# Performance work log

Measured on AMD Instinct MI355X. Metric: run time of the kernel, lower is better.

## Reference

```python
import jax, jax.numpy as jnp
import numpy as np

N_HEAD = 16

def setup_inputs() -> dict:
    key = jax.random.key(0)
    k1, k2, k3, k4, k5 = jax.random.split(key, 5)
    B, S, D = 2, 2048, 1024
    return {
        "hidden_states": jax.random.normal(k1, (B, S, D), jnp.float32),
        "w_attn": jax.random.normal(k2, (D, 3 * D), jnp.float32) * 0.02,
        "b_attn": jax.random.normal(k3, (3 * D,), jnp.float32) * 0.02,
        "w_proj": jax.random.normal(k4, (D, D), jnp.float32) * 0.02,
        "b_proj": jax.random.normal(k5, (D,), jnp.float32) * 0.02,
    }

def reference(hidden_states, w_attn, b_attn, w_proj, b_proj):
    B, S, D = hidden_states.shape
    H = N_HEAD
    Dh = D // H
    qkv = hidden_states @ w_attn + b_attn              # [B,S,3D]
    q, k, v = jnp.split(qkv, 3, axis=-1)
    def split_heads(x):
        return x.reshape(B, S, H, Dh).transpose(0, 2, 1, 3)  # [B,H,S,Dh]
    q, k, v = split_heads(q), split_heads(k), split_heads(v)
    # scale=True: divide by sqrt(head_dim) (v.size(-1))
    scores = jnp.einsum("bhqd,bhkd->bhqk", q, k) / jnp.sqrt(jnp.float32(Dh))
    attn = jax.nn.softmax(scores, axis=-1)             # [B,H,S,S]
    out = jnp.einsum("bhqk,bhkd->bhqd", attn, v)       # [B,H,S,Dh]
    out = out.transpose(0, 2, 1, 3).reshape(B, S, D)   # merge heads
    return out @ w_proj + b_proj
```

## Files before the change

### kernel.cpp

```cpp
#include <hip/hip_runtime.h>
#include <hip/hip_bf16.h>

typedef __attribute__((ext_vector_type(8))) short bf16x8;
typedef __attribute__((ext_vector_type(4))) float f32x4;
typedef __attribute__((ext_vector_type(16))) float f32x16;

#define LOG2E 1.4426950408889634f
#define SCALE_F (0.125f * LOG2E)

__device__ inline unsigned short f2bf(float f) {
  union { float f; unsigned u; } x; x.f = f;
  unsigned u = x.u;
  unsigned r = u + 0x7FFFu + ((u >> 16) & 1u);
  return (unsigned short)(r >> 16);
}

__device__ inline unsigned cvtpk(float lo, float hi) {
  unsigned r;
  asm("v_cvt_pk_bf16_f32 %0, %1, %2" : "=v"(r) : "v"(lo), "v"(hi));
  return r;
}

__device__ inline void gload16(const unsigned short* g, unsigned short* l) {
  __builtin_amdgcn_global_load_lds(
      (const __attribute__((address_space(1))) unsigned int*)g,
      (__attribute__((address_space(3))) unsigned int*)l, 16, 0, 0);
}

template <int J>
__device__ inline bf16x8 pack_pfrag(f32x16 p) {
  int X, Y, Z, W;
  asm("v_cvt_pk_bf16_f32 %0, %1, %2" : "=v"(X) : "v"(p[J + 0]), "v"(p[J + 1]));
  asm("v_cvt_pk_bf16_f32 %0, %1, %2" : "=v"(Y) : "v"(p[J + 2]), "v"(p[J + 3]));
  asm("v_cvt_pk_bf16_f32 %0, %1, %2" : "=v"(Z) : "v"(p[J + 4]), "v"(p[J + 5]));
  asm("v_cvt_pk_bf16_f32 %0, %1, %2" : "=v"(W) : "v"(p[J + 6]), "v"(p[J + 7]));
  asm("v_permlane32_swap_b32 %0, %1" : "+v"(X), "+v"(Z));
  asm("v_permlane32_swap_b32 %0, %1" : "+v"(Y), "+v"(W));
  union { int w[4]; bf16x8 v; } u;
  u.w[0] = X; u.w[1] = Y; u.w[2] = Z; u.w[3] = W;
  return u.v;
}

__device__ inline void transpose_tile(const float* __restrict__ W,
                                      unsigned short* __restrict__ WT, int K, int N,
                                      int n0, int k0, int t,
                                      unsigned short (*Tl)[72]) {
#pragma unroll
  for (int i = 0; i < 4; ++i) {
    int idx = t + i * 256;
    int r = idx >> 4, c4 = (idx & 15) << 2;
    float4 v = *reinterpret_cast<const float4*>(&W[(size_t)(k0 + r) * N + n0 + c4]);
    Tl[c4 + 0][r] = f2bf(v.x);
    Tl[c4 + 1][r] = f2bf(v.y);
    Tl[c4 + 2][r] = f2bf(v.z);
    Tl[c4 + 3][r] = f2bf(v.w);
  }
  __syncthreads();
#pragma unroll
  for (int i = 0; i < 2; ++i) {
    int idx = t + i * 256;
    int rr = idx >> 3, cc = (idx & 7) << 3;
    *reinterpret_cast<int4*>(&WT[(size_t)(n0 + rr) * K + k0 + cc]) =
        *reinterpret_cast<const int4*>(&Tl[rr][cc]);
  }
}

__global__ __launch_bounds__(256) void prep_fused(
    const float* __restrict__ hs, unsigned short* __restrict__ hs_b,
    const float* __restrict__ w_attn, unsigned short* __restrict__ wT,
    const float* __restrict__ w_proj, unsigned short* __restrict__ pT) {
  __shared__ unsigned short Tl[64][72];
  const int bid = blockIdx.x, t = threadIdx.x;
  if (bid < 768) {
    transpose_tile(w_attn, wT, 1024, 3072, (bid % 48) * 64, (bid / 48) * 64, t, Tl);
  } else if (bid < 1024) {
    int r = bid - 768;
    transpose_tile(w_proj, pT, 1024, 1024, (r % 16) * 64, (r / 16) * 64, t, Tl);
  } else {
    int cb = bid - 1024;
#pragma unroll
    for (int j = 0; j < 4; ++j) {
      int i = cb * 1024 + j * 256 + t;
      float4 v = reinterpret_cast<const float4*>(hs)[i];
      ushort4 o;
      o.x = f2bf(v.x); o.y = f2bf(v.y); o.z = f2bf(v.z); o.w = f2bf(v.w);
      reinterpret_cast<ushort4*>(hs_b)[i] = o;
    }
  }
}

__global__ __launch_bounds__(512, 2) void gemm_qkv_8p(
    const unsigned short* __restrict__ A, const unsigned short* __restrict__ Bt,
    const float* __restrict__ bias,
    unsigned short* __restrict__ qw, unsigned short* __restrict__ kw,
    unsigned short* __restrict__ vtg) {
  __shared__ unsigned short Abuf[2][16384];
  __shared__ unsigned short Bbuf[2][12288];
  const int t = threadIdx.x, lane = t & 63, wid = t >> 6;
  const int wm = wid >> 2, wn = wid & 3;
  const int orig = blockIdx.x;
  const int nid = (orig & 7) * 32 + (orig >> 3);
  const int mt = nid >> 4, nt = nid & 15;
  const int row0 = mt * 256, col0 = nt * 192;
  const int lr = lane & 15, kq = lane >> 4;
  const int srow_lo = lane >> 3;
  const int scg = (lane & 7) ^ srow_lo;
  const unsigned short* Ab = A + (size_t)row0 * 1024;
  const unsigned short* Bb = Bt + (size_t)col0 * 1024;
  f32x4 acc[8][3] = {};

#define SA8(bs, kt)                                                              \
  {                                                                              \
    const unsigned short* Ap = Ab + (kt) * 64;                                   \
    _Pragma("unroll") for (int i = 0; i < 4; ++i) {                              \
      int g = wid * 4 + i;                                                       \
      int rrel = g * 8 + srow_lo;                                                \
      gload16(&Ap[(size_t)rrel * 1024 + scg * 8], &Abuf[bs][g * 512]);           \
    }                                                                            \
  }
#define SB8(bs, kt)                                                              \
  {                                                                              \
    const unsigned short* Bp = Bb + (kt) * 64;                                   \
    _Pragma("unroll") for (int i = 0; i < 3; ++i) {                              \
      int g = wid * 3 + i;                                                       \
      int rrel = g * 8 + srow_lo;                                                \
      gload16(&Bp[(size_t)rrel * 1024 + scg * 8], &Bbuf[bs][g * 512]);           \
    }                                                                            \
  }
#define RDA(dst, mh)                                                             \
  _Pragma("unroll") for (int m = 0; m < 4; ++m)                                  \
  _Pragma("unroll") for (int ks = 0; ks < 2; ++ks) {                             \
    int row = wm * 128 + (mh) * 64 + m * 16 + lr;                                \
    dst[m][ks] = *reinterpret_cast<const bf16x8*>(                               \
        &Ac[row * 64 + (((ks * 4 + kq) ^ (row & 7)) << 3)]);                     \
  }
#define RDB2(dst)                                                                \
  _Pragma("unroll") for (int n = 0; n < 2; ++n)                                  \
  _Pragma("unroll") for (int ks = 0; ks < 2; ++ks) {                             \
    int row = wn * 48 + n * 16 + lr;                                             \
    dst[n][ks] = *reinterpret_cast<const bf16x8*>(                               \
        &Bc[row * 64 + (((ks * 4 + kq) ^ (row & 7)) << 3)]);                     \
  }
#define RDB1(dst)                                                                \
  _Pragma("unroll") for (int ks = 0; ks < 2; ++ks) {                             \
    int row = wn * 48 + 32 + lr;                                                 \
    dst[0][ks] = *reinterpret_cast<const bf16x8*>(                               \
        &Bc[row * 64 + (((ks * 4 + kq) ^ (row & 7)) << 3)]);                     \
  }
#define QMM2(mh, afv, bfv)                                                       \
  _Pragma("unroll") for (int m = 0; m < 4; ++m)                                  \
  _Pragma("unroll") for (int n = 0; n < 2; ++n)                                  \
  _Pragma("unroll") for (int ks = 0; ks < 2; ++ks)                               \
    acc[(mh) * 4 + m][n] = __builtin_amdgcn_mfma_f32_16x16x32_bf16(              \
        afv[m][ks], bfv[n][ks], acc[(mh) * 4 + m][n], 0, 0, 0);
#define QMM1(mh, afv, bfv)                                                       \
  _Pragma("unroll") for (int m = 0; m < 4; ++m)                                  \
  _Pragma("unroll") for (int ks = 0; ks < 2; ++ks)                               \
    acc[(mh) * 4 + m][2] = __builtin_amdgcn_mfma_f32_16x16x32_bf16(              \
        afv[m][ks], bfv[0][ks], acc[(mh) * 4 + m][2], 0, 0, 0);
#define BAR8 __builtin_amdgcn_s_barrier();

  SA8(0, 0) SB8(0, 0)
  asm volatile("s_waitcnt vmcnt(0)" ::: "memory");
  BAR8
  __builtin_amdgcn_sched_barrier(0);

  for (int kt = 0; kt < 16; ++kt) {
    const int buf = kt & 1;
    const unsigned short* Ac = Abuf[buf];
    const unsigned short* Bc = Bbuf[buf];
    bf16x8 af0[4][2], af1[4][2], bf0[2][2], bf1[1][2];
    RDA(af0, 0) RDB2(bf0)
    if (kt < 15) SA8(buf ^ 1, kt + 1)
    BAR8
    __builtin_amdgcn_s_setprio(1); QMM2(0, af0, bf0) __builtin_amdgcn_s_setprio(0);
    BAR8
    RDA(af1, 1)
    if (kt < 15) SB8(buf ^ 1, kt + 1)
    BAR8
    __builtin_amdgcn_s_setprio(1); QMM2(1, af1, bf0) __builtin_amdgcn_s_setprio(0);
    BAR8
    RDB1(bf1)
    BAR8
    __builtin_amdgcn_s_setprio(1); QMM1(0, af0, bf1) __builtin_amdgcn_s_setprio(0);
    BAR8
    __builtin_amdgcn_s_setprio(1); QMM1(1, af1, bf1) __builtin_amdgcn_s_setprio(0);
    if (kt < 15) { asm volatile("s_waitcnt vmcnt(0)" ::: "memory"); }
    BAR8
    __builtin_amdgcn_sched_barrier(0);
  }
#undef SA8
#undef SB8
#undef RDA
#undef RDB2
#undef RDB1
#undef QMM2
#undef QMM1
#undef BAR8

  const int rbase = (lane >> 4) * 4;
#pragma unroll
  for (int mm = 0; mm < 8; ++mm) {
#pragma unroll
    for (int nn = 0; nn < 3; ++nn) {
      int c = col0 + wn * 48 + nn * 16 + lr;
      int which = c >> 10;
      int d = c & 1023;
      int h = d >> 6, dh = d & 63;
      float bv = bias[c];
      int m0 = row0 + wm * 128 + mm * 16 + rbase;
      int b = m0 >> 11, s0 = m0 & 2047;
      if (which == 2) {
        int kt = s0 >> 6, key0 = s0 & 63;
        ushort4 pv;
        pv.x = f2bf(acc[mm][nn][0] + bv);
        pv.y = f2bf(acc[mm][nn][1] + bv);
        pv.z = f2bf(acc[mm][nn][2] + bv);
        pv.w = f2bf(acc[mm][nn][3] + bv);
        *reinterpret_cast<ushort4*>(
            &vtg[(((size_t)(b * 16 + h) * 32 + kt) * 64 + dh) * 64 + key0]) = pv;
      } else if (which == 1) {
#pragma unroll
        for (int r = 0; r < 4; ++r)
          kw[(((size_t)b * 16 + h) * 2048 + (s0 + r)) * 64 + dh] = f2bf(acc[mm][nn][r] + bv);
      } else {
#pragma unroll
        for (int r = 0; r < 4; ++r)
          qw[(((size_t)b * 16 + h) * 2048 + (s0 + r)) * 64 + dh] =
              f2bf((acc[mm][nn][r] + bv) * SCALE_F);
      }
    }
  }
}

__global__ __launch_bounds__(512, 4) void gemm_proj_8p(
    const unsigned short* __restrict__ A, const unsigned short* __restrict__ Bt,
    const float* __restrict__ bias, float* __restrict__ out) {
  __shared__ unsigned short Abuf[2][8192];
  __shared__ unsigned short Bbuf[2][8192];
  const int t = threadIdx.x, lane = t & 63, wid = t >> 6;
  const int wm = wid >> 2, wn = wid & 3;
  const int orig = blockIdx.x;
  const int nid = (orig & 7) * 32 + (orig >> 3);
  const int row0 = (nid >> 3) * 128, col0 = (nid & 7) * 128;
  const int lr = lane & 15, kq = lane >> 4;
  const int srow_lo = lane >> 3;
  const int scg = (lane & 7) ^ srow_lo;
  const unsigned short* Ab = A + (size_t)row0 * 1024;
  const unsigned short* Bb = Bt + (size_t)col0 * 1024;
  f32x4 acc[4][2] = {};

#define SP(bs, kt)                                                               \
  {                                                                              \
    const unsigned short* Ap = Ab + (kt) * 64;                                   \
    const unsigned short* Bp = Bb + (kt) * 64;                                   \
    _Pragma("unroll") for (int i = 0; i < 2; ++i) {                              \
      int g = wid * 2 + i;                                                       \
      int rrel = g * 8 + srow_lo;                                                \
      gload16(&Ap[(size_t)rrel * 1024 + scg * 8], &Abuf[bs][g * 512]);           \
      gload16(&Bp[(size_t)rrel * 1024 + scg * 8], &Bbuf[bs][g * 512]);           \
    }                                                                            \
  }
#define RPA(dst, mh)                                                             \
  _Pragma("unroll") for (int m = 0; m < 2; ++m)                                  \
  _Pragma("unroll") for (int ks = 0; ks < 2; ++ks) {                             \
    int row = wm * 64 + (mh) * 32 + m * 16 + lr;                                 \
    dst[m][ks] = *reinterpret_cast<const bf16x8*>(                               \
        &Ac[row * 64 + (((ks * 4 + kq) ^ (row & 7)) << 3)]);                     \
  }
#define RPB(dst)                                                                 \
  _Pragma("unroll") for (int n = 0; n < 2; ++n)                                  \
  _Pragma("unroll") for (int ks = 0; ks < 2; ++ks) {                             \
    int row = wn * 32 + n * 16 + lr;                                             \
    dst[n][ks] = *reinterpret_cast<const bf16x8*>(                               \
        &Bc[row * 64 + (((ks * 4 + kq) ^ (row & 7)) << 3)]);                     \
  }
#define PMM(mh, afv, bfv)                                                        \
  _Pragma("unroll") for (int m = 0; m < 2; ++m)                                  \
  _Pragma("unroll") for (int n = 0; n < 2; ++n)                                  \
  _Pragma("unroll") for (int ks = 0; ks < 2; ++ks)                               \
    acc[(mh) * 2 + m][n] = __builtin_amdgcn_mfma_f32_16x16x32_bf16(              \
        afv[m][ks], bfv[n][ks], acc[(mh) * 2 + m][n], 0, 0, 0);
#define BARP __builtin_amdgcn_s_barrier();

  SP(0, 0)
  asm volatile("s_waitcnt vmcnt(0)" ::: "memory");
  BARP
  __builtin_amdgcn_sched_barrier(0);

  for (int kt = 0; kt < 16; ++kt) {
    const int buf = kt & 1;
    const unsigned short* Ac = Abuf[buf];
    const unsigned short* Bc = Bbuf[buf];
    bf16x8 af0[2][2], af1[2][2], bfv[2][2];
    RPA(af0, 0) RPB(bfv)
    if (kt < 15) SP(buf ^ 1, kt + 1)
    BARP
    __builtin_amdgcn_s_setprio(1); PMM(0, af0, bfv) __builtin_amdgcn_s_setprio(0);
    BARP
    RPA(af1, 1)
    BARP
    __builtin_amdgcn_s_setprio(1); PMM(1, af1, bfv) __builtin_amdgcn_s_setprio(0);
    if (kt < 15) { asm volatile("s_waitcnt vmcnt(0)" ::: "memory"); }
    BARP
    __builtin_amdgcn_sched_barrier(0);
  }
#undef SP
#undef RPA
#undef RPB
#undef PMM
#undef BARP

  const int rbase = (lane >> 4) * 4;
#pragma unroll
  for (int mm = 0; mm < 4; ++mm) {
#pragma unroll
    for (int nn = 0; nn < 2; ++nn) {
      int c = col0 + wn * 32 + nn * 16 + lr;
      float bv = bias[c];
#pragma unroll
      for (int r = 0; r < 4; ++r) {
        int m = row0 + wm * 64 + mm * 16 + rbase + r;
        out[(size_t)m * 1024 + c] = acc[mm][nn][r] + bv;
      }
    }
  }
}

__global__ __launch_bounds__(512, 4) void attn_kernel(
    const unsigned short* __restrict__ qw, const unsigned short* __restrict__ kw,
    const unsigned short* __restrict__ vtg, unsigned short* __restrict__ ow) {
  __shared__ char smem[65536];
  unsigned short* KV = (unsigned short*)smem;
  unsigned short* Ol = (unsigned short*)smem;
  float* EX = (float*)(smem + 18432);
  const int t = threadIdx.x, lane = t & 63, wid = t >> 6;
  const int half = wid >> 2, wq = wid & 3;
  const int l31 = lane & 31, hi = lane >> 5;
  const int orig = blockIdx.x + 16 * blockIdx.y;
  const int nid = (orig & 7) * 64 + (orig >> 3);
  const int qt = nid & 15, bh = nid >> 4;
  const int b = bh >> 4, h = bh & 15;
  const unsigned short* Qg = qw + (size_t)bh * 2048 * 64;
  const unsigned short* Kg = kw + (size_t)bh * 2048 * 64;
  const unsigned short* Vg = vtg + (size_t)bh * 32 * 4096;
  const int q0 = qt * 128 + wq * 32;

  bf16x8 qf[4];
#pragma unroll
  for (int kc = 0; kc < 4; ++kc)
    qf[kc] = *reinterpret_cast<const bf16x8*>(&Qg[(q0 + l31) * 64 + kc * 16 + hi * 8]);

  f32x16 oA = {0,0,0,0,0,0,0,0,0,0,0,0,0,0,0,0};
  f32x16 oB = {0,0,0,0,0,0,0,0,0,0,0,0,0,0,0,0};
  float lrun = 0.f;

  const int srow_lo = lane >> 3;
  const int scg0 = (lane & 7) ^ srow_lo;
  const int rsw = (l31 & 7) ^ ((l31 >> 3) & 3);

#define STAGE(buf, kt)                                                              \
  {                                                                                 \
    const unsigned short* Kt = Kg + (size_t)(kt) * 4096;                            \
    const unsigned short* Vs = Vg + (size_t)(kt) * 4096;                            \
    unsigned short* Kl = KV + half * 16384 + (buf) * 8192;                          \
    unsigned short* Vl = Kl + 4096;                                                 \
    _Pragma("unroll") for (int i = 0; i < 2; ++i) {                                 \
      int chunk = wq * 2 + i;                                                       \
      int row = chunk * 8 + srow_lo;                                                \
      int sc = (scg0 ^ (chunk & 3)) * 8;                                            \
      gload16(&Kt[row * 64 + sc], &Kl[chunk * 512]);                                \
      gload16(&Vs[row * 64 + sc], &Vl[chunk * 512]);                                \
    }                                                                               \
  }

  const int kt0 = half * 16;
  STAGE(0, kt0)

  for (int it = 0; it < 16; ++it) {
    const int cur = it & 1;
    asm volatile("s_waitcnt vmcnt(0)" ::: "memory");
    __builtin_amdgcn_s_barrier();
    if (it + 1 < 16) STAGE(cur ^ 1, kt0 + it + 1)
    const unsigned short* Kl = KV + half * 16384 + cur * 8192;
    const unsigned short* Vl = Kl + 4096;

    f32x16 sA = {0,0,0,0,0,0,0,0,0,0,0,0,0,0,0,0};
    f32x16 sB = {0,0,0,0,0,0,0,0,0,0,0,0,0,0,0,0};
    __builtin_amdgcn_s_setprio(1);
#pragma unroll
    for (int kc = 0; kc < 4; ++kc) {
      bf16x8 k0f = *reinterpret_cast<const bf16x8*>(
          &Kl[l31 * 64 + (((kc * 2 + hi) ^ rsw) << 3)]);
      bf16x8 k1f = *reinterpret_cast<const bf16x8*>(
          &Kl[(32 + l31) * 64 + (((kc * 2 + hi) ^ rsw) << 3)]);
      sA = __builtin_amdgcn_mfma_f32_32x32x16_bf16(k0f, qf[kc], sA, 0, 0, 0);
      sB = __builtin_amdgcn_mfma_f32_32x32x16_bf16(k1f, qf[kc], sB, 0, 0, 0);
    }
    __builtin_amdgcn_s_setprio(0);

    float rsv[16];
#pragma unroll
    for (int j = 0; j < 16; ++j) {
      float pa = exp2f(sA[j]);
      float pb = exp2f(sB[j]);
      sA[j] = pa; sB[j] = pb;
      rsv[j] = pa + pb;
    }
#pragma unroll
    for (int s = 8; s >= 1; s >>= 1)
#pragma unroll
      for (int j = 0; j < s; ++j) rsv[j] += rsv[j + s];
    lrun += rsv[0] + __shfl_xor(rsv[0], 32);

    bf16x8 pf0 = pack_pfrag<0>(sA);
    bf16x8 pf1 = pack_pfrag<8>(sA);
    bf16x8 pf2 = pack_pfrag<0>(sB);
    bf16x8 pf3 = pack_pfrag<8>(sB);

    __builtin_amdgcn_s_setprio(1);
#pragma unroll
    for (int c = 0; c < 4; ++c) {
      bf16x8 pf = (c == 0) ? pf0 : (c == 1) ? pf1 : (c == 2) ? pf2 : pf3;
      int g = c * 2 + hi;
      bf16x8 v0f = *reinterpret_cast<const bf16x8*>(
          &Vl[l31 * 64 + ((g ^ rsw) << 3)]);
      bf16x8 v1f = *reinterpret_cast<const bf16x8*>(
          &Vl[(32 + l31) * 64 + ((g ^ rsw) << 3)]);
      oA = __builtin_amdgcn_mfma_f32_32x32x16_bf16(v0f, pf, oA, 0, 0, 0);
      oB = __builtin_amdgcn_mfma_f32_32x32x16_bf16(v1f, pf, oB, 0, 0, 0);
    }
    __builtin_amdgcn_s_setprio(0);
  }
#undef STAGE

  __syncthreads();
  if (half == 1) {
    float* e = EX + ((size_t)(wq * 64 + lane)) * 34;
#pragma unroll
    for (int j = 0; j < 16; ++j) { e[j] = oA[j]; e[16 + j] = oB[j]; }
    e[32] = lrun;
  }
  __syncthreads();
  if (half == 0) {
    const float* e = EX + ((size_t)(wq * 64 + lane)) * 34;
    float linv = 1.0f / (lrun + e[32]);
    unsigned short* orow_l = Ol + (wq * 32 + l31) * 72;
#pragma unroll
    for (int g = 0; g < 4; ++g) {
      float a0 = (oA[4 * g + 0] + e[4 * g + 0]) * linv;
      float a1v = (oA[4 * g + 1] + e[4 * g + 1]) * linv;
      float a2v = (oA[4 * g + 2] + e[4 * g + 2]) * linv;
      float a3v = (oA[4 * g + 3] + e[4 * g + 3]) * linv;
      uint2 w0; w0.x = cvtpk(a0, a1v); w0.y = cvtpk(a2v, a3v);
      *reinterpret_cast<uint2*>(&orow_l[8 * g + 4 * hi]) = w0;
      float b0 = (oB[4 * g + 0] + e[16 + 4 * g + 0]) * linv;
      float b1v = (oB[4 * g + 1] + e[16 + 4 * g + 1]) * linv;
      float b2v = (oB[4 * g + 2] + e[16 + 4 * g + 2]) * linv;
      float b3v = (oB[4 * g + 3] + e[16 + 4 * g + 3]) * linv;
      uint2 w1; w1.x = cvtpk(b0, b1v); w1.y = cvtpk(b2v, b3v);
      *reinterpret_cast<uint2*>(&orow_l[32 + 8 * g + 4 * hi]) = w1;
    }
  }
  __syncthreads();
#pragma unroll
  for (int i = 0; i < 2; ++i) {
    int idx = t + i * 512;
    int q = idx >> 3, ch = idx & 7;
    int4 v = *reinterpret_cast<const int4*>(&Ol[q * 72 + ch * 8]);
    *reinterpret_cast<int4*>(
        &ow[(((size_t)b * 2048 + qt * 128 + q) * 16 + h) * 64 + ch * 8]) = v;
  }
}

extern "C" void kernel_launch(void* const* d_in, const int* in_sizes, int n_in,
                              void* d_out, int out_size, void* d_ws, size_t ws_size,
                              hipStream_t stream) {
  const float* hs = (const float*)d_in[0];
  const float* w_attn = (const float*)d_in[1];
  const float* b_attn = (const float*)d_in[2];
  const float* w_proj = (const float*)d_in[3];
  const float* b_proj = (const float*)d_in[4];
  float* out = (float*)d_out;

  const size_t HEAD = (size_t)2 * 16 * 2048 * 64;
  unsigned short* qw = (unsigned short*)d_ws;
  unsigned short* kw = qw + HEAD;
  unsigned short* vtg = kw + HEAD;
  unsigned short* hs_b = vtg + HEAD;
  unsigned short* ow = hs_b;
  unsigned short* wT = hs_b + HEAD;
  unsigned short* pT = wT + (size_t)3072 * 1024;

  prep_fused<<<dim3(2048), 256, 0, stream>>>(hs, hs_b, w_attn, wT, w_proj, pT);

  gemm_qkv_8p<<<dim3(256), 512, 0, stream>>>(hs_b, wT, b_attn, qw, kw, vtg);
  attn_kernel<<<dim3(16, 32), 512, 0, stream>>>(qw, kw, vtg, ow);
  gemm_proj_8p<<<dim3(256), 512, 0, stream>>>(ow, pT, b_proj, out);
}
```

Before: 114.9 us.

## Drop split-KV halves in attention; each block handles 256 queries over full KV

Previously each attention block split the key range between two 4-wave halves and merged partial outputs through shared memory. Now all 8 waves share one K/V stream, each wave owning 32 of 256 query rows and iterating all 32 key tiles. This removes the cross-half merge, an extra barrier and the exchange buffer, halves K/V global loads per query and cuts LDS use. The cost is half as many blocks (256 instead of 512) and twice as many serial iterations per block, so the GPU runs fewer workgroups.

```diff
diff --git a/kernel.cpp b/kernel.cpp
--- a/kernel.cpp
+++ b/kernel.cpp
@@ -330,21 +330,19 @@
 __global__ __launch_bounds__(512, 4) void attn_kernel(
     const unsigned short* __restrict__ qw, const unsigned short* __restrict__ kw,
     const unsigned short* __restrict__ vtg, unsigned short* __restrict__ ow) {
-  __shared__ char smem[65536];
+  __shared__ char smem[36864];
   unsigned short* KV = (unsigned short*)smem;
   unsigned short* Ol = (unsigned short*)smem;
-  float* EX = (float*)(smem + 18432);
   const int t = threadIdx.x, lane = t & 63, wid = t >> 6;
-  const int half = wid >> 2, wq = wid & 3;
   const int l31 = lane & 31, hi = lane >> 5;
-  const int orig = blockIdx.x + 16 * blockIdx.y;
-  const int nid = (orig & 7) * 64 + (orig >> 3);
-  const int qt = nid & 15, bh = nid >> 4;
+  const int orig = blockIdx.x + 8 * blockIdx.y;
+  const int nid = (orig & 7) * 32 + (orig >> 3);
+  const int qt = nid & 7, bh = nid >> 3;
   const int b = bh >> 4, h = bh & 15;
   const unsigned short* Qg = qw + (size_t)bh * 2048 * 64;
   const unsigned short* Kg = kw + (size_t)bh * 2048 * 64;
   const unsigned short* Vg = vtg + (size_t)bh * 32 * 4096;
-  const int q0 = qt * 128 + wq * 32;
+  const int q0 = qt * 256 + wid * 32;
 
   bf16x8 qf[4];
 #pragma unroll
@@ -363,26 +361,22 @@
   {                                                                                 \
     const unsigned short* Kt = Kg + (size_t)(kt) * 4096;                            \
     const unsigned short* Vs = Vg + (size_t)(kt) * 4096;                            \
-    unsigned short* Kl = KV + half * 16384 + (buf) * 8192;                          \
+    unsigned short* Kl = KV + (buf) * 8192;                                         \
     unsigned short* Vl = Kl + 4096;                                                 \
-    _Pragma("unroll") for (int i = 0; i < 2; ++i) {                                 \
-      int chunk = wq * 2 + i;                                                       \
-      int row = chunk * 8 + srow_lo;                                                \
-      int sc = (scg0 ^ (chunk & 3)) * 8;                                            \
-      gload16(&Kt[row * 64 + sc], &Kl[chunk * 512]);                                \
-      gload16(&Vs[row * 64 + sc], &Vl[chunk * 512]);                                \
-    }                                                                               \
-  }
-
-  const int kt0 = half * 16;
-  STAGE(0, kt0)
-
-  for (int it = 0; it < 16; ++it) {
+    int row = wid * 8 + srow_lo;                                                    \
+    int sc = (scg0 ^ (wid & 3)) * 8;                                                \
+    gload16(&Kt[row * 64 + sc], &Kl[wid * 512]);                                    \
+    gload16(&Vs[row * 64 + sc], &Vl[wid * 512]);                                    \
+  }
+
+  STAGE(0, 0)
+
+  for (int it = 0; it < 32; ++it) {
     const int cur = it & 1;
     asm volatile("s_waitcnt vmcnt(0)" ::: "memory");
     __builtin_amdgcn_s_barrier();
-    if (it + 1 < 16) STAGE(cur ^ 1, kt0 + it + 1)
-    const unsigned short* Kl = KV + half * 16384 + cur * 8192;
+    if (it + 1 < 32) STAGE(cur ^ 1, it + 1)
+    const unsigned short* Kl = KV + cur * 8192;
     const unsigned short* Vl = Kl + 4096;
 
     f32x16 sA = {0,0,0,0,0,0,0,0,0,0,0,0,0,0,0,0};
@@ -435,41 +429,29 @@
 #undef STAGE
 
   __syncthreads();
-  if (half == 1) {
-    float* e = EX + ((size_t)(wq * 64 + lane)) * 34;
-#pragma unroll
-    for (int j = 0; j < 16; ++j) { e[j] = oA[j]; e[16 + j] = oB[j]; }
-    e[32] = lrun;
+  {
+    float linv = 1.0f / lrun;
+    unsigned short* orow_l = Ol + (wid * 32 + l31) * 72;
+#pragma unroll
+    for (int g = 0; g < 4; ++g) {
+      uint2 w0;
+      w0.x = cvtpk(oA[4 * g + 0] * linv, oA[4 * g + 1] * linv);
+      w0.y = cvtpk(oA[4 * g + 2] * linv, oA[4 * g + 3] * linv);
+      *reinterpret_cast<uint2*>(&orow_l[8 * g + 4 * hi]) = w0;
+      uint2 w1;
+      w1.x = cvtpk(oB[4 * g + 0] * linv, oB[4 * g + 1] * linv);
+      w1.y = cvtpk(oB[4 * g + 2] * linv, oB[4 * g + 3] * linv);
+      *reinterpret_cast<uint2*>(&orow_l[32 + 8 * g + 4 * hi]) = w1;
+    }
   }
   __syncthreads();
-  if (half == 0) {
-    const float* e = EX + ((size_t)(wq * 64 + lane)) * 34;
-    float linv = 1.0f / (lrun + e[32]);
-    unsigned short* orow_l = Ol + (wq * 32 + l31) * 72;
-#pragma unroll
-    for (int g = 0; g < 4; ++g) {
-      float a0 = (oA[4 * g + 0] + e[4 * g + 0]) * linv;
-      float a1v = (oA[4 * g + 1] + e[4 * g + 1]) * linv;
-      float a2v = (oA[4 * g + 2] + e[4 * g + 2]) * linv;
-      float a3v = (oA[4 * g + 3] + e[4 * g + 3]) * linv;
-      uint2 w0; w0.x = cvtpk(a0, a1v); w0.y = cvtpk(a2v, a3v);
-      *reinterpret_cast<uint2*>(&orow_l[8 * g + 4 * hi]) = w0;
-      float b0 = (oB[4 * g + 0] + e[16 + 4 * g + 0]) * linv;
-      float b1v = (oB[4 * g + 1] + e[16 + 4 * g + 1]) * linv;
-      float b2v = (oB[4 * g + 2] + e[16 + 4 * g + 2]) * linv;
-      float b3v = (oB[4 * g + 3] + e[16 + 4 * g + 3]) * linv;
-      uint2 w1; w1.x = cvtpk(b0, b1v); w1.y = cvtpk(b2v, b3v);
-      *reinterpret_cast<uint2*>(&orow_l[32 + 8 * g + 4 * hi]) = w1;
-    }
-  }
-  __syncthreads();
-#pragma unroll
-  for (int i = 0; i < 2; ++i) {
+#pragma unroll
+  for (int i = 0; i < 4; ++i) {
     int idx = t + i * 512;
     int q = idx >> 3, ch = idx & 7;
     int4 v = *reinterpret_cast<const int4*>(&Ol[q * 72 + ch * 8]);
     *reinterpret_cast<int4*>(
-        &ow[(((size_t)b * 2048 + qt * 128 + q) * 16 + h) * 64 + ch * 8]) = v;
+        &ow[(((size_t)b * 2048 + qt * 256 + q) * 16 + h) * 64 + ch * 8]) = v;
   }
 }
 
@@ -495,6 +477,6 @@
   prep_fused<<<dim3(2048), 256, 0, stream>>>(hs, hs_b, w_attn, wT, w_proj, pT);
 
   gemm_qkv_8p<<<dim3(256), 512, 0, stream>>>(hs_b, wT, b_attn, qw, kw, vtg);
-  attn_kernel<<<dim3(16, 32), 512, 0, stream>>>(qw, kw, vtg, ow);
+  attn_kernel<<<dim3(8, 32), 512, 0, stream>>>(qw, kw, vtg, ow);
   gemm_proj_8p<<<dim3(256), 512, 0, stream>>>(ow, pT, b_proj, out);
 }
```

New measurement: 116.6 us. Within noise of the previous version (+1.5%).
